# Kernel tuning notes

Measured on AMD Instinct MI355X. Metric: run time of the kernel, lower is better.

The kernel has to match this reference:

```python
import jax, jax.numpy as jnp
import numpy as np

EPS = 1e-5
ALPHA = 0.05   # propalpha
GDEP = 2       # gcn_depth
LAYERS = 3     # gcn_layers
NUM_TCN = 2    # num_layer tcn units per encoder


def conv1x1(W, b, x):
    # 1x1 Conv2d on [B,C,N,1]: pure channel mix
    return jnp.einsum('oc,bcnl->bonl', W, x) + b[None, :, None, None]


def tcn_unit(Wf, bf, Wg, bg, h):
    # gated TCN unit: tanh(filter) * sigmoid(gate), 1x1 convs (L==1)
    return jnp.tanh(conv1x1(Wf, bf, h)) * jax.nn.sigmoid(conv1x1(Wg, bg, h))


def mixprop(x, A, W, b):
    # MTGNN mixprop: add self-loops, row-normalize, gdep propagation steps,
    # concat hops on channel dim, 1x1 conv mlp. A: [N,N] or [B,N,N].
    N = A.shape[-1]
    A = A + jnp.eye(N, dtype=A.dtype)
    A = A / A.sum(-1, keepdims=True)
    h = x
    outs = [h]
    for _ in range(GDEP):
        if A.ndim == 2:
            hn = jnp.einsum('vw,bcwl->bcvl', A, h)
        else:
            hn = jnp.einsum('bvw,bcwl->bcvl', A, h)
        h = ALPHA * x + (1.0 - ALPHA) * hn
        outs.append(h)
    ho = jnp.concatenate(outs, axis=1)  # [B,(GDEP+1)*C,N,1]
    return conv1x1(W, b, ho)


def layernorm(x, w, b):
    # LayerNorm over (C,N,1) of [B,C,N,1]; idx=arange(N) selects full affine
    mu = x.mean(axis=(1, 2, 3), keepdims=True)
    var = x.var(axis=(1, 2, 3), keepdims=True)
    return (x - mu) / jnp.sqrt(var + EPS) * w[None] + b[None]


def setup_inputs() -> dict:
    key = jax.random.key(0)
    B, N, E, H, S, T = 8, 2048, 32, 128, 256, 12
    ks = jax.random.split(key, 32)
    s = 0.05
    inp = {
        'x': jax.random.normal(ks[0], (B, E, N, 1), jnp.float32),
        'dy_graph': jax.random.uniform(ks[1], (B, N, N), jnp.float32),
        'static_graph': jax.random.uniform(ks[2], (N, N), jnp.float32),
        'spatial_emb': jax.random.normal(ks[3], (B, 32, N, 1), jnp.float32),
        'temporal_d_emb': jax.random.normal(ks[4], (B, 32, N, 1), jnp.float32),
        'temporal_w_emb': jax.random.normal(ks[5], (B, 32, N, 1), jnp.float32),
        'enc_Wf': s * jax.random.normal(ks[6], (LAYERS, NUM_TCN, H, H), jnp.float32),
        'enc_bf': s * jax.random.normal(ks[7], (LAYERS, NUM_TCN, H), jnp.float32),
        'enc_Wg': s * jax.random.normal(ks[8], (LAYERS, NUM_TCN, H, H), jnp.float32),
        'enc_bg': s * jax.random.normal(ks[9], (LAYERS, NUM_TCN, H), jnp.float32),
        'skip_W': s * jax.random.normal(ks[10], (LAYERS, S, H), jnp.float32),
        'skip_b': s * jax.random.normal(ks[11], (LAYERS, S), jnp.float32),
        'norm_w': jnp.ones((LAYERS, E, N, 1), jnp.float32),
        'norm_b': jnp.zeros((LAYERS, E, N, 1), jnp.float32),
        'g0_W': s * jax.random.normal(ks[12], (LAYERS, E, (GDEP + 1) * E), jnp.float32),
        'g0_b': s * jax.random.normal(ks[13], (LAYERS, E), jnp.float32),
        'g1_W': s * jax.random.normal(ks[14], (LAYERS, E, (GDEP + 1) * E), jnp.float32),
        'g1_b': s * jax.random.normal(ks[15], (LAYERS, E), jnp.float32),
        'g2_W': s * jax.random.normal(ks[16], (LAYERS, E, (GDEP + 1) * E), jnp.float32),
        'g2_b': s * jax.random.normal(ks[17], (LAYERS, E), jnp.float32),
        'skipE_W': s * jax.random.normal(ks[18], (S, E), jnp.float32),
        'skipE_b': s * jax.random.normal(ks[19], (S,), jnp.float32),
        'end_W': s * jax.random.normal(ks[20], (T, S), jnp.float32),
        'end_b': s * jax.random.normal(ks[21], (T,), jnp.float32),
    }
    return inp


def reference(x, dy_graph, static_graph, spatial_emb, temporal_d_emb, temporal_w_emb,
              enc_Wf, enc_bf, enc_Wg, enc_bg, skip_W, skip_b, norm_w, norm_b,
              g0_W, g0_b, g1_W, g1_b, g2_W, g2_b, skipE_W, skipE_b, end_W, end_b):
    adp = dy_graph
    skip = 0.0
    for i in range(LAYERS):
        residual = x
        hidden = jnp.concatenate([x, spatial_emb, temporal_d_emb, temporal_w_emb], axis=1)
        for j in range(NUM_TCN):
            hidden = tcn_unit(enc_Wf[i, j], enc_bf[i, j], enc_Wg[i, j], enc_bg[i, j], hidden)
        skip = conv1x1(skip_W[i], skip_b[i], hidden) + skip
        x = (mixprop(x, static_graph, g0_W[i], g0_b[i])
             + mixprop(x, adp, g1_W[i], g1_b[i])
             + mixprop(x, jnp.swapaxes(adp, -1, -2), g2_W[i], g2_b[i]))
        x = x + residual
        x = jax.nn.relu(layernorm(x, norm_w[i], norm_b[i]))
    skip = conv1x1(skipE_W, skipE_b, x) + skip
    return conv1x1(end_W, end_b, skip)  # [B, seq_length, N, 1]
```

## Files before the change

### kernel.cpp

```cpp
#include <hip/hip_runtime.h>
#include <stdint.h>


typedef uint16_t u16;
typedef uint32_t u32;
typedef __attribute__((ext_vector_type(8))) short s8v;
typedef __attribute__((ext_vector_type(4))) float f4v;

#define MFMA16(a,b,c) __builtin_amdgcn_mfma_f32_16x16x32_bf16(a,b,c,0,0,0)

__device__ __forceinline__ float b2f(u16 u){ union{u32 i; float f;} x; x.i=(u32)u<<16; return x.f; }
__device__ __forceinline__ u16 f2b(float f){
  u32 u = __builtin_bit_cast(u32, f);
  u32 r = (u + 0x7fffu + ((u >> 16) & 1u)) >> 16;
  return (u16)r;
}

__device__ __forceinline__ void gld16(const void* g, void* l) {
  __builtin_amdgcn_global_load_lds(
      (const __attribute__((address_space(1))) void*)g,
      (__attribute__((address_space(3))) void*)l, 16, 0, 0);
}

__global__ __launch_bounds__(256) void kdetect(const u16* __restrict__ x, int* __restrict__ flag)
{
  const int i = blockIdx.x*256 + threadIdx.x;
  const uint4 v = ((const uint4*)x)[i];
  const u32 w[4] = {v.x, v.y, v.z, v.w};
  int cnt = 0;
  #pragma unroll
  for (int e = 0; e < 4; e++) {
    if ((w[e] & 0x7F80u) == 0x7F80u) cnt++;
    if (((w[e] >> 16) & 0x7F80u) == 0x7F80u) cnt++;
  }
  const unsigned long long m = __ballot(cnt != 0);
  if (m && (threadIdx.x & 63) == 0) atomicOr(flag, 1);
}

__global__ __launch_bounds__(256) void kcvt4(const void* __restrict__ src, u16* __restrict__ dst,
                                             int n4, const int* __restrict__ flag)
{
  if (!*flag) return;
  const int i = blockIdx.x*256 + threadIdx.x;
  if (i >= n4) return;
  const float4 v = ((const float4*)src)[i];
  u16 o[4]; o[0]=f2b(v.x); o[1]=f2b(v.y); o[2]=f2b(v.z); o[3]=f2b(v.w);
  *(uint2*)(dst + (long)i*4) = *(uint2*)o;
}

struct CvtTab { const void* s[18]; u16* d[18]; int n4[18]; };
__global__ __launch_bounds__(256) void kcvt_small(CvtTab tb, const int* __restrict__ flag)
{
  const int e = blockIdx.y;
  const int i = blockIdx.x*256 + threadIdx.x;
  if (i >= tb.n4[e]) return;
  if (*flag) {
    const float4 v = ((const float4*)tb.s[e])[i];
    u16 o[4]; o[0]=f2b(v.x); o[1]=f2b(v.y); o[2]=f2b(v.z); o[3]=f2b(v.w);
    *(uint2*)(tb.d[e] + (long)i*4) = *(uint2*)o;
  } else {
    *(uint2*)(tb.d[e] + (long)i*4) = ((const uint2*)tb.s[e])[i];
  }
}

__global__ __launch_bounds__(256) void kcvtT(
    const void* __restrict__ src, u16* __restrict__ dyb, u16* __restrict__ dytb,
    float* __restrict__ rsum, float* __restrict__ csum, const int* __restrict__ flag)
{
  __shared__ alignas(16) u32 tt[64][32];
  const int tid = threadIdx.x;
  const int b = blockIdx.z;
  const long r0 = (long)blockIdx.y*64;
  const long c0 = (long)blockIdx.x*64;
  const int rp = tid>>3, c8 = (tid&7)*8;
  const long base = (long)b*4194304;
  const int fl = *flag;

  u16 lo[8], hi[8];
  const long gl = base + (r0 + 2*rp)*2048 + c0 + c8;
  const long gh = gl + 2048;
  if (fl) {
    const float* sl = (const float*)src + gl;
    const float* sh = (const float*)src + gh;
    const float4 a0 = ((const float4*)sl)[0], a1 = ((const float4*)sl)[1];
    const float4 b0 = ((const float4*)sh)[0], b1 = ((const float4*)sh)[1];
    lo[0]=f2b(a0.x); lo[1]=f2b(a0.y); lo[2]=f2b(a0.z); lo[3]=f2b(a0.w);
    lo[4]=f2b(a1.x); lo[5]=f2b(a1.y); lo[6]=f2b(a1.z); lo[7]=f2b(a1.w);
    hi[0]=f2b(b0.x); hi[1]=f2b(b0.y); hi[2]=f2b(b0.z); hi[3]=f2b(b0.w);
    hi[4]=f2b(b1.x); hi[5]=f2b(b1.y); hi[6]=f2b(b1.z); hi[7]=f2b(b1.w);
    *(uint4*)(dyb + gl) = *(uint4*)lo;
    *(uint4*)(dyb + gh) = *(uint4*)hi;
  } else {
    *(uint4*)lo = *((const uint4*)((const u16*)src + gl));
    *(uint4*)hi = *((const uint4*)((const u16*)src + gh));
  }
  float rsl = 0.f, rsh = 0.f;
  #pragma unroll
  for (int e = 0; e < 8; e++) {
    rsl += b2f(lo[e]); rsh += b2f(hi[e]);
    const int c = c8 + e;
    tt[c][rp ^ ((c & 0x38) >> 1)] = (u32)lo[e] | ((u32)hi[e] << 16);
  }
  rsl += __shfl_down(rsl, 4, 8); rsl += __shfl_down(rsl, 2, 8); rsl += __shfl_down(rsl, 1, 8);
  rsh += __shfl_down(rsh, 4, 8); rsh += __shfl_down(rsh, 2, 8); rsh += __shfl_down(rsh, 1, 8);
  if ((tid & 7) == 0) {
    atomicAdd(rsum + b*2048 + r0 + 2*rp,     rsl);
    atomicAdd(rsum + b*2048 + r0 + 2*rp + 1, rsh);
  }
  __syncthreads();

  const int c = tid>>2, j4 = (tid&3)*8;
  const int sw = (c & 0x38) >> 1;
  u32 q[8];
  *(uint4*)&q[0] = *(const uint4*)&tt[c][j4 ^ sw];
  *(uint4*)&q[4] = *(const uint4*)&tt[c][(j4 + 4) ^ sw];
  float cs = 0.f;
  #pragma unroll
  for (int e = 0; e < 8; e++) { cs += b2f((u16)q[e]); cs += b2f((u16)(q[e] >> 16)); }
  cs += __shfl_down(cs, 2, 4); cs += __shfl_down(cs, 1, 4);
  u16* dp = dytb + base + (c0 + c)*2048 + r0 + 2*j4;
  *(uint4*)(dp)     = *(uint4*)&q[0];
  *(uint4*)(dp + 8) = *(uint4*)&q[4];
  if ((tid & 3) == 0) atomicAdd(csum + b*2048 + c0 + c, cs);
}

__global__ void kfin(float* __restrict__ v){
  const int i = blockIdx.x*256 + threadIdx.x;
  v[i] = 1.f/(1.f + v[i]);
}

struct PG {
  const u16* Ac0; const u16* Ac1; const u16* Ac2;
  const u16* Ar0; const u16* Ar1;
  const int* flag;
  long ab0, ab1, ab2;
  const u16* X0; const u16* X1; const u16* X2;
  const float* R0; const float* R1; const float* R2;
  long rb0, rb1, rb2;
  u16* O0; u16* O1; u16* O2;
};

__global__ __launch_bounds__(256) void kprops(PG p, long x_bs, long o_bs)
{
  __shared__ u16 Al[4][64][64];
  __shared__ u16 Xl[4][32][64];
  const int tid = threadIdx.x, wave = tid>>6, lane = tid&63;
  const int lw = lane&15, quad = lane>>4;
  const int wr = wave>>1, wc = wave&1;
  const int v0 = blockIdx.x*64;
  const int b = blockIdx.y, g = blockIdx.z;
  const int fl = *p.flag;
  const u16* Ag; long ab; const u16* Xg; const float* Rg; long rb; u16* Og;
  if (g == 0)      { Ag = fl ? p.Ac0 : p.Ar0; ab = p.ab0; Xg = p.X0; Rg = p.R0; rb = p.rb0; Og = p.O0; }
  else if (g == 1) { Ag = fl ? p.Ac1 : p.Ar1; ab = p.ab1; Xg = p.X1; Rg = p.R1; rb = p.rb1; Og = p.O1; }
  else             { Ag = p.Ac2;              ab = p.ab2; Xg = p.X2; Rg = p.R2; rb = p.rb2; Og = p.O2; }
  const u16* Ab = Ag + (long)b*ab;
  const u16* Xb = Xg + (long)b*x_bs;

  const int srow = wave*8 + (lane>>3);
  const int skc  = lane&7;
  const long soff = (long)((skc ^ (srow&7))*8);
  const u16* srcA0 = Ab + (long)(v0 + srow)*2048 + soff;
  const u16* srcA1 = Ab + (long)(v0 + 32 + srow)*2048 + soff;
  const u16* srcX  = Xb + (long)srow*2048 + soff;

#define STAGE(tt) do { const int bb_=(tt)&3; const long k0_=(long)(tt)*64;          \
    gld16(srcA0 + k0_, (void*)((char*)&Al[bb_][0][0]  + wave*1024));                \
    gld16(srcA1 + k0_, (void*)((char*)&Al[bb_][32][0] + wave*1024));                \
    gld16(srcX  + k0_, (void*)((char*)&Xl[bb_][0][0]  + wave*1024)); } while(0)

  f4v acc0 = {0.f,0.f,0.f,0.f}, acc1 = {0.f,0.f,0.f,0.f};
  const int arow0 = wr*32 + lw;
  const int arow1 = wr*32 + 16 + lw;
  const int xrow  = wc*16 + lw;
  const int sw    = lw & 7;
  const int q0    = (quad ^ sw)*8;
  const int q1    = ((quad ^ sw) ^ 4)*8;

  STAGE(0); STAGE(1); STAGE(2);

  #pragma unroll 1
  for (int t = 0; t < 32; t++) {
    if (t < 30)       asm volatile("s_waitcnt vmcnt(6)" ::: "memory");
    else if (t == 30) asm volatile("s_waitcnt vmcnt(3)" ::: "memory");
    else              asm volatile("s_waitcnt vmcnt(0)" ::: "memory");
    __builtin_amdgcn_s_barrier();
    __builtin_amdgcn_sched_barrier(0);
    const int bb = t&3;
    s8v x0  = *(const s8v*)&Xl[bb][xrow][q0];
    s8v a00 = *(const s8v*)&Al[bb][arow0][q0];
    s8v a10 = *(const s8v*)&Al[bb][arow1][q0];
    s8v x1  = *(const s8v*)&Xl[bb][xrow][q1];
    s8v a01 = *(const s8v*)&Al[bb][arow0][q1];
    s8v a11 = *(const s8v*)&Al[bb][arow1][q1];
    acc0 = MFMA16(a00, x0, acc0);
    acc1 = MFMA16(a10, x0, acc1);
    acc0 = MFMA16(a01, x1, acc0);
    acc1 = MFMA16(a11, x1, acc1);
    if (t <= 28) STAGE(t+3);
  }
#undef STAGE

  const int c = wc*16 + lw;
  const float* rp = Rg + (long)b*rb;
  u16* ob = Og + (long)b*o_bs;
  #pragma unroll
  for (int f = 0; f < 2; f++) {
    const f4v s = f ? acc1 : acc0;
    const int vb = v0 + wr*32 + f*16 + quad*4;
    const u16* dp = Xb + (long)c*2048 + vb;
    u16 pk[4];
    #pragma unroll
    for (int r = 0; r < 4; r++) pk[r] = f2b((s[r] + b2f(dp[r])) * rp[vb + r]);
    *(uint2*)(ob + (long)c*2048 + vb) = *(uint2*)pk;
  }
}

template<int TRANSA, int MODE>
__global__ __launch_bounds__(256) void kprop(
    const u16* __restrict__ A, long a_bs, int lda, int K,
    const u16* __restrict__ X, long x_bs, int ldx,
    const u16* __restrict__ D, long d_bs,
    const float* __restrict__ rinv, long r_bs,
    const float* __restrict__ bias,
    u16* __restrict__ out0, float* __restrict__ out1, long o_bs,
    float* __restrict__ stats)
{
  __shared__ u16 As[4][2][16][40];
  __shared__ f4v red[4][2][64];
  const int tid = threadIdx.x;
  const int wave = tid >> 6, lane = tid & 63;
  const int lw = lane & 15, quad = lane >> 4;
  const int v0 = blockIdx.x * 16;
  const int ball = blockIdx.z + blockIdx.y;
  const u16* Ab = A + (long)ball * a_bs;
  const u16* Xb = X + (long)ball * x_bs;
  const int KC = K >> 5;

  f4v acc0 = {0.f,0.f,0.f,0.f}, acc1 = {0.f,0.f,0.f,0.f};

  int r0, c0_;
  if (TRANSA == 0) { r0 = lane >> 2; c0_ = (lane & 3) * 8; }
  else             { r0 = lane >> 1; c0_ = (lane & 1) * 8; }

  int ci = wave;
  bool has = ci < KC;
  uint4 d = make_uint4(0,0,0,0);
  if (has) {
    d = (TRANSA == 0)
      ? *(const uint4*)(Ab + (long)(v0 + r0) * lda + ci * 32 + c0_)
      : *(const uint4*)(Ab + (long)(ci * 32 + r0) * lda + v0 + c0_);
  }
  int buf = 0;
  while (has) {
    if (TRANSA == 0) {
      *(uint4*)&As[wave][buf][r0][c0_] = d;
    } else {
      u16 tmp[8]; *(uint4*)tmp = d;
      #pragma unroll
      for (int e = 0; e < 8; e++) As[wave][buf][c0_ + e][r0] = tmp[e];
    }
    const int cn = ci + 4;
    const bool hn = cn < KC;
    if (hn) {
      d = (TRANSA == 0)
        ? *(const uint4*)(Ab + (long)(v0 + r0) * lda + cn * 32 + c0_)
        : *(const uint4*)(Ab + (long)(cn * 32 + r0) * lda + v0 + c0_);
    }
    s8v af = *(const s8v*)&As[wave][buf][lw][quad * 8];
    const u16* xk = Xb + ci * 32 + quad * 8;
    s8v b0 = *(const s8v*)(xk + (long)lw * ldx);
    s8v b1 = *(const s8v*)(xk + (long)(16 + lw) * ldx);
    acc0 = MFMA16(af, b0, acc0);
    acc1 = MFMA16(af, b1, acc1);
    ci = cn; has = hn; buf ^= 1;
  }
  red[wave][0][lane] = acc0;
  red[wave][1][lane] = acc1;
  __syncthreads();
  if (wave == 0) {
    const int vb = v0 + quad * 4;
    float ssum = 0.f, sq = 0.f;
    #pragma unroll
    for (int nt = 0; nt < 2; nt++) {
      f4v a = red[0][nt][lane] + red[1][nt][lane] + red[2][nt][lane] + red[3][nt][lane];
      const int c = nt * 16 + lw;
      const u16* dp = D + (long)ball * d_bs + (long)c * 2048 + vb;
      if (MODE == 0) {
        const float* rp = rinv + (long)ball * r_bs + vb;
        u16 pk[4];
        #pragma unroll
        for (int r = 0; r < 4; r++) pk[r] = f2b((a[r] + b2f(dp[r])) * rp[r]);
        *(uint2*)(out0 + (long)ball * o_bs + (long)c * 2048 + vb) = *(uint2*)pk;
      } else {
        const float bs = bias[c];
        float4 st;
        st.x = a[0] + bs + b2f(dp[0]);
        st.y = a[1] + bs + b2f(dp[1]);
        st.z = a[2] + bs + b2f(dp[2]);
        st.w = a[3] + bs + b2f(dp[3]);
        *(float4*)(out1 + (long)ball * o_bs + (long)c * 2048 + vb) = st;
        ssum += st.x + st.y + st.z + st.w;
        sq   += st.x*st.x + st.y*st.y + st.z*st.z + st.w*st.w;
      }
    }
    if (MODE == 1) {
      #pragma unroll
      for (int off = 32; off; off >>= 1) {
        ssum += __shfl_down(ssum, off, 64);
        sq   += __shfl_down(sq,   off, 64);
      }
      if (lane == 0) {
        atomicAdd(stats + ball*2,     ssum);
        atomicAdd(stats + ball*2 + 1, sq);
      }
    }
  }
}

__global__ __launch_bounds__(256) void ktcn2(
    const u16* __restrict__ H,
    const u16* __restrict__ Wf1, const u16* __restrict__ bf1v,
    const u16* __restrict__ Wg1, const u16* __restrict__ bg1v,
    const u16* __restrict__ Wf2, const u16* __restrict__ bf2v,
    const u16* __restrict__ Wg2, const u16* __restrict__ bg2v,
    u16* __restrict__ out)
{
  __shared__ u16 h1[4][16][136];
  const int tid = threadIdx.x, wave = tid>>6, lane = tid&63, lw = lane&15, quad = lane>>4;
  const long j0 = (long)blockIdx.x*64 + wave*16;
  const f4v zero = {0.f,0.f,0.f,0.f};
  f4v accf[8], accg[8];
  #pragma unroll
  for (int nt=0; nt<8; nt++){ accf[nt] = zero; accg[nt] = zero; }
  const u16* Arow = H + (j0 + lw)*128 + quad*8;
  #pragma unroll
  for (int k0 = 0; k0 < 128; k0 += 32) {
    s8v a = *(const s8v*)(Arow + k0);
    #pragma unroll
    for (int nt = 0; nt < 8; nt++) {
      const int o = nt*16 + lw;
      s8v bf_ = *(const s8v*)(Wf1 + o*128 + k0 + quad*8);
      s8v bg_ = *(const s8v*)(Wg1 + o*128 + k0 + quad*8);
      accf[nt] = MFMA16(a, bf_, accf[nt]);
      accg[nt] = MFMA16(a, bg_, accg[nt]);
    }
  }
  #pragma unroll
  for (int nt = 0; nt < 8; nt++) {
    const int o = nt*16 + lw;
    const float fb = b2f(bf1v[o]), gb = b2f(bg1v[o]);
    #pragma unroll
    for (int rr = 0; rr < 4; rr++) {
      const float f = accf[nt][rr] + fb, g = accg[nt][rr] + gb;
      const float e2 = __expf(2.f*f);
      const float th = 1.f - 2.f/(e2 + 1.f);
      const float sg = 1.f/(1.f + __expf(-g));
      h1[wave][quad*4 + rr][o] = f2b(th*sg);
    }
  }
  __syncthreads();
  #pragma unroll
  for (int nt=0; nt<8; nt++){ accf[nt] = zero; accg[nt] = zero; }
  #pragma unroll
  for (int k0 = 0; k0 < 128; k0 += 32) {
    s8v a = *(const s8v*)&h1[wave][lw][k0 + quad*8];
    #pragma unroll
    for (int nt = 0; nt < 8; nt++) {
      const int o = nt*16 + lw;
      s8v bf_ = *(const s8v*)(Wf2 + o*128 + k0 + quad*8);
      s8v bg_ = *(const s8v*)(Wg2 + o*128 + k0 + quad*8);
      accf[nt] = MFMA16(a, bf_, accf[nt]);
      accg[nt] = MFMA16(a, bg_, accg[nt]);
    }
  }
  #pragma unroll
  for (int nt = 0; nt < 8; nt++) {
    const int o = nt*16 + lw;
    const float fb = b2f(bf2v[o]), gb = b2f(bg2v[o]);
    #pragma unroll
    for (int rr = 0; rr < 4; rr++) {
      const long j = j0 + quad*4 + rr;
      const float f = accf[nt][rr] + fb, g = accg[nt][rr] + gb;
      const float e2 = __expf(2.f*f);
      const float th = 1.f - 2.f/(e2 + 1.f);
      const float sg = 1.f/(1.f + __expf(-g));
      out[j*128 + o] = f2b(th*sg);
    }
  }
}

__global__ __launch_bounds__(256) void kskip(
    const u16* __restrict__ A, int lda, int K,
    const u16* __restrict__ W, int ldb,
    const u16* __restrict__ bias,
    float* __restrict__ skipbuf, int addprev, int mode, u16* __restrict__ outb)
{
  const int tid = threadIdx.x, wave = tid>>6, lane = tid&63, lw = lane&15, quad = lane>>4;
  const long j0 = (long)blockIdx.x*64 + wave*16;
  const f4v zero = {0.f,0.f,0.f,0.f};
  f4v acc[16];
  #pragma unroll
  for (int nt=0; nt<16; nt++) acc[nt] = zero;
  const u16* Arow = A + (j0 + lw)*(long)lda + quad*8;
  for (int k0 = 0; k0 < K; k0 += 32) {
    s8v a = *(const s8v*)(Arow + k0);
    #pragma unroll
    for (int nt = 0; nt < 16; nt++) {
      const int o = nt*16 + lw;
      s8v b = *(const s8v*)(W + (long)o*ldb + k0 + quad*8);
      acc[nt] = MFMA16(a, b, acc[nt]);
    }
  }
  #pragma unroll
  for (int nt = 0; nt < 16; nt++) {
    const int o = nt*16 + lw;
    const float bv = b2f(bias[o]);
    #pragma unroll
    for (int rr = 0; rr < 4; rr++) {
      const long j = j0 + quad*4 + rr;
      float v = acc[nt][rr] + bv;
      if (addprev) v += skipbuf[j*256 + o];
      if (mode == 0) skipbuf[j*256 + o] = v;
      else           outb[j*256 + o] = f2b(v);
    }
  }
}

__global__ __launch_bounds__(256) void kend(
    const u16* __restrict__ A, const u16* __restrict__ W, const u16* __restrict__ bias,
    void* __restrict__ outv, const int* __restrict__ flag)
{
  const int tid = threadIdx.x, wave = tid>>6, lane = tid&63, lw = lane&15, quad = lane>>4;
  const long j0 = (long)blockIdx.x*64 + wave*16;
  f4v acc = {0.f,0.f,0.f,0.f};
  const u16* Arow = A + (j0 + lw)*256 + quad*8;
  #pragma unroll
  for (int k0 = 0; k0 < 256; k0 += 32) {
    s8v a = *(const s8v*)(Arow + k0);
    s8v b = {0,0,0,0,0,0,0,0};
    if (lw < 12) b = *(const s8v*)(W + lw*256 + k0 + quad*8);
    acc = MFMA16(a, b, acc);
  }
  if (lw < 12) {
    const float bv = b2f(bias[lw]);
    const int fl = *flag;
    #pragma unroll
    for (int rr = 0; rr < 4; rr++) {
      const long j = j0 + quad*4 + rr;
      const long oi = (j >> 11)*24576 + lw*2048 + (j & 2047);
      const float val = acc[rr] + bv;
      if (fl) ((float*)outv)[oi] = val;
      else    ((u16*)outv)[oi]   = f2b(val);
    }
  }
}

__global__ __launch_bounds__(256) void khid0(
    const void* __restrict__ x, const void* __restrict__ spat,
    const void* __restrict__ tde, const void* __restrict__ twe,
    u16* __restrict__ hid, u16* __restrict__ slot0, const int* __restrict__ flag)
{
  __shared__ u16 t[32][72];
  const int tid = threadIdx.x, b = blockIdx.y, v0 = blockIdx.x*64;
  const int fl = *flag;
  const void* srcs[4] = {x, spat, tde, twe};
  #pragma unroll
  for (int e = 0; e < 4; e++) {
    const int c = tid>>3, v8 = (tid&7)*8;
    const long boff = (long)c*2048 + v0 + v8;
    u16 o8[8];
    if (fl) {
      const float* sp = (const float*)srcs[e] + (long)b*65536 + boff;
      const float4 a = ((const float4*)sp)[0], bb = ((const float4*)sp)[1];
      o8[0]=f2b(a.x); o8[1]=f2b(a.y); o8[2]=f2b(a.z); o8[3]=f2b(a.w);
      o8[4]=f2b(bb.x); o8[5]=f2b(bb.y); o8[6]=f2b(bb.z); o8[7]=f2b(bb.w);
    } else {
      *(uint4*)o8 = *(const uint4*)((const u16*)srcs[e] + (long)b*65536 + boff);
    }
    if (e == 0) *(uint4*)(slot0 + (long)b*458752 + boff) = *(uint4*)o8;
    *(uint4*)&t[c][v8] = *(uint4*)o8;
    __syncthreads();
    const int jl = tid>>2, c8 = (tid&3)*8;
    u16 q8[8];
    #pragma unroll
    for (int i = 0; i < 8; i++) q8[i] = t[c8 + i][jl];
    *(uint4*)(hid + ((long)b*2048 + v0 + jl)*128 + e*32 + c8) = *(uint4*)q8;
    __syncthreads();
  }
}

__global__ __launch_bounds__(256) void krowsum(const u16* __restrict__ srcA, const u16* __restrict__ srcB,
                                               const int* __restrict__ flag,
                                               float* __restrict__ outv, int nrows)
{
  const u16* src = (*flag) ? srcA : srcB;
  const int wave = threadIdx.x>>6, lane = threadIdx.x&63;
  const int row = blockIdx.x*4 + wave;
  if (row >= nrows) return;
  const u16* p = src + (long)row*2048 + lane*8;
  float s = 0.f;
  #pragma unroll
  for (int it = 0; it < 4; it++) {
    u16 v[8]; *(uint4*)v = *(const uint4*)(p + it*512);
    #pragma unroll
    for (int e = 0; e < 8; e++) s += b2f(v[e]);
  }
  #pragma unroll
  for (int off = 32; off; off >>= 1) s += __shfl_down(s, off, 64);
  if (lane == 0) outv[row] = 1.f/(1.f + s);
}

__global__ __launch_bounds__(256) void kweff(
    const u16* __restrict__ g0W, const u16* __restrict__ g1W, const u16* __restrict__ g2W,
    const u16* __restrict__ g0b, const u16* __restrict__ g1b, const u16* __restrict__ g2b,
    u16* __restrict__ weffA, float* __restrict__ bwA)
{
  const int L = blockIdx.y;
  const int ioff = L*3072, boff = L*32;
  u16* weff = weffA + L*7168;
  float* bw = bwA + L*32;
  const int idx = blockIdx.x*256 + threadIdx.x;
  if (idx < 32) bw[idx] = b2f(g0b[boff+idx]) + b2f(g1b[boff+idx]) + b2f(g2b[boff+idx]);
  if (idx >= 7168) return;
  const int o = idx / 224, m = idx % 224;
  const u16* Ws[3] = {g0W + ioff, g1W + ioff, g2W + ioff};
  float val;
  if (m < 32) {
    val = 0.f;
    #pragma unroll
    for (int g = 0; g < 3; g++) {
      const float w0 = b2f(Ws[g][o*96 + m]);
      const float w1 = b2f(Ws[g][o*96 + 32 + m]);
      const float w2 = b2f(Ws[g][o*96 + 64 + m]);
      val += w0 + 0.05f*(w1 + w2);
    }
  } else {
    const int f = (m - 32) >> 5, cc = m & 31;
    const int g = f >> 1, typ = f & 1;
    const float w1 = b2f(Ws[g][o*96 + 32 + cc]);
    const float w2 = b2f(Ws[g][o*96 + 64 + cc]);
    val = (typ == 0) ? (0.95f*w1 + 0.0475f*w2) : (0.9025f*w2);
  }
  weff[o*224 + m] = f2b(val);
}

__global__ __launch_bounds__(256) void kapply(
    const float* __restrict__ xpre, const float* __restrict__ raw,
    const u16* __restrict__ nw, const u16* __restrict__ nb,
    u16* __restrict__ slot0, u16* __restrict__ hid)
{
  __shared__ u16 t[32][72];
  const int tid = threadIdx.x, b = blockIdx.y, v0 = blockIdx.x*64;
  const float mu = raw[b*2] * (1.f/65536.f);
  const float var = raw[b*2+1] * (1.f/65536.f) - mu*mu;
  const float rs = rsqrtf(var + 1e-5f);
  const int c = tid>>3, v8 = (tid&7)*8;
  const long boff = (long)c*2048 + v0 + v8;
  float4 xa = *(const float4*)(xpre + (long)b*65536 + boff);
  float4 xbv = *(const float4*)(xpre + (long)b*65536 + boff + 4);
  u16 wv[8], bv[8], o8[8];
  *(uint4*)wv = *(const uint4*)(nw + boff);
  *(uint4*)bv = *(const uint4*)(nb + boff);
  const float xs[8] = {xa.x, xa.y, xa.z, xa.w, xbv.x, xbv.y, xbv.z, xbv.w};
  #pragma unroll
  for (int e = 0; e < 8; e++) {
    float y = (xs[e] - mu) * rs * b2f(wv[e]) + b2f(bv[e]);
    y = fmaxf(y, 0.f);
    o8[e] = f2b(y);
    t[c][v8 + e] = o8[e];
  }
  *(uint4*)(slot0 + (long)b*458752 + boff) = *(uint4*)o8;
  __syncthreads();
  const int jl = tid>>2, c8 = (tid&3)*8;
  u16 q8[8];
  #pragma unroll
  for (int e = 0; e < 8; e++) q8[e] = t[c8 + e][jl];
  *(uint4*)(hid + ((long)b*2048 + v0 + jl)*128 + c8) = *(uint4*)q8;
}

extern "C" void kernel_launch(void* const* d_in, const int* in_sizes, int n_in,
                              void* d_out, int out_size, void* d_ws, size_t ws_size,
                              hipStream_t stream)
{
  (void)in_sizes; (void)n_in; (void)out_size; (void)ws_size;

  char* ws = (char*)d_ws;
  u16*   pbuf = (u16*)(ws + 0);
  u16*   hid  = (u16*)(ws + 7340032);
  u16*   hb2  = (u16*)(ws + 15728640);
  float* skip = (float*)(ws + 19922944);
  u16*   xsb  = (u16*)(ws + 36700160);
  float* xpre = (float*)(ws + 45088768);
  float* rst  = (float*)(ws + 47203328);
  float* rdy  = (float*)(ws + 47211520);
  float* cdy  = (float*)(ws + 47277056);
  int*   flag = (int*)(ws + 47343616);
  float* raw  = (float*)(ws + 47343744);

  size_t coff = 50331648;
  auto alloc = [&](size_t elems) -> u16* {
    u16* p = (u16*)(ws + coff);
    coff += ((elems*2 + 255)/256)*256;
    return p;
  };
  u16* dyb   = alloc(33554432);
  u16* stgb  = alloc(4194304);
  u16* encWf = alloc(98304);
  u16* encbf = alloc(768);
  u16* encWg = alloc(98304);
  u16* encbg = alloc(768);
  u16* skW   = alloc(98304);
  u16* skb   = alloc(768);
  u16* nw    = alloc(196608);
  u16* nb    = alloc(196608);
  u16* g0W   = alloc(9216);
  u16* g0b   = alloc(96);
  u16* g1W   = alloc(9216);
  u16* g1b   = alloc(96);
  u16* g2W   = alloc(9216);
  u16* g2b   = alloc(96);
  u16* sEW   = alloc(8192);
  u16* sEb   = alloc(256);
  u16* eW    = alloc(3072);
  u16* eb    = alloc(12);
  u16* dytb  = alloc(33554432);
  u16* weffA = alloc(21504);
  float* bwA = (float*)alloc(192);

  hipMemsetAsync(flag, 0, 320, stream);
  hipLaunchKernelGGL(kdetect, dim3(32), dim3(256), 0, stream, (const u16*)d_in[0], flag);

  CvtTab tb;
  {
    const void* ss[18] = { d_in[6], d_in[7], d_in[8], d_in[9], d_in[10], d_in[11],
      d_in[12], d_in[13], d_in[14], d_in[15], d_in[16], d_in[17], d_in[18], d_in[19],
      d_in[20], d_in[21], d_in[22], d_in[23] };
    u16* dd[18] = { encWf, encbf, encWg, encbg, skW, skb, nw, nb,
      g0W, g0b, g1W, g1b, g2W, g2b, sEW, sEb, eW, eb };
    const int nn[18] = { 24576, 192, 24576, 192, 24576, 192, 49152, 49152,
      2304, 24, 2304, 24, 2304, 24, 2048, 64, 768, 3 };
    for (int e = 0; e < 18; e++) { tb.s[e] = ss[e]; tb.d[e] = dd[e]; tb.n4[e] = nn[e]; }
  }
  hipLaunchKernelGGL(kcvt_small, dim3(192, 18), dim3(256), 0, stream, tb, flag);
  hipLaunchKernelGGL(kcvt4, dim3(4096), dim3(256), 0, stream, d_in[2], stgb, 1048576, flag);
  hipLaunchKernelGGL(kweff, dim3(28, 3), dim3(256), 0, stream,
      g0W, g1W, g2W, g0b, g1b, g2b, weffA, bwA);

  hipMemsetAsync(rdy, 0, 131072, stream);
  hipLaunchKernelGGL(kcvtT, dim3(32,32,8), dim3(256), 0, stream,
      d_in[1], dyb, dytb, rdy, cdy, flag);
  hipLaunchKernelGGL(kfin, dim3(128), dim3(256), 0, stream, rdy);
  hipLaunchKernelGGL(krowsum, dim3(512), dim3(256), 0, stream,
      stgb, (const u16*)d_in[2], flag, rst, 2048);
  hipLaunchKernelGGL(khid0, dim3(32,8), dim3(256), 0, stream,
      d_in[0], d_in[3], d_in[4], d_in[5], hid, pbuf, flag);

  const long PB = 458752;
  const long SL = 65536;
  const long DYB = 4194304;

  for (int i = 0; i < 3; i++) {
    hipLaunchKernelGGL(ktcn2, dim3(256), dim3(256), 0, stream,
        hid,
        encWf + (i*2+0)*16384, encbf + (i*2+0)*128, encWg + (i*2+0)*16384, encbg + (i*2+0)*128,
        encWf + (i*2+1)*16384, encbf + (i*2+1)*128, encWg + (i*2+1)*16384, encbg + (i*2+1)*128,
        hb2);
    hipLaunchKernelGGL(kskip, dim3(256), dim3(256), 0, stream,
        hb2, 128, 128, skW + i*32768, 128, skb + i*256, skip, (i>0)?1:0, 0, (u16*)nullptr);

    PG p1;
    p1.Ac0 = stgb; p1.Ac1 = dyb; p1.Ac2 = dytb;
    p1.Ar0 = (const u16*)d_in[2]; p1.Ar1 = (const u16*)d_in[1];
    p1.flag = flag;
    p1.ab0 = 0;   p1.ab1 = DYB; p1.ab2 = DYB;
    p1.X0 = pbuf; p1.X1 = pbuf; p1.X2 = pbuf;
    p1.R0 = rst;  p1.R1 = rdy;  p1.R2 = cdy;
    p1.rb0 = 0;   p1.rb1 = 2048; p1.rb2 = 2048;
    p1.O0 = pbuf + 1*SL; p1.O1 = pbuf + 3*SL; p1.O2 = pbuf + 5*SL;
    hipLaunchKernelGGL(kprops, dim3(32,8,3), dim3(256), 0, stream, p1, PB, PB);

    PG p2 = p1;
    p2.X0 = pbuf + 1*SL; p2.X1 = pbuf + 3*SL; p2.X2 = pbuf + 5*SL;
    p2.O0 = pbuf + 2*SL; p2.O1 = pbuf + 4*SL; p2.O2 = pbuf + 6*SL;
    hipLaunchKernelGGL(kprops, dim3(32,8,3), dim3(256), 0, stream, p2, PB, PB);

    hipLaunchKernelGGL((kprop<1,1>), dim3(128,1,8), dim3(256), 0, stream,
        pbuf, PB, 2048, 224, weffA + i*7168, 0L, 224, pbuf, PB,
        (const float*)nullptr, 0L, bwA + i*32, (u16*)nullptr, xpre, 65536L, raw + i*16);
    hipLaunchKernelGGL(kapply, dim3(32,8), dim3(256), 0, stream,
        xpre, raw + i*16, nw + i*65536, nb + i*65536, pbuf, hid);
  }
  hipLaunchKernelGGL(kskip, dim3(256), dim3(256), 0, stream,
      hid, 128, 32, sEW, 32, sEb, skip, 1, 1, xsb);
  hipLaunchKernelGGL(kend, dim3(256), dim3(256), 0, stream, xsb, eW, eb, d_out, flag);
}
```

Before: 773.3 us.

## Unfuse the two TCN units and widen kcvtT tiles to 128 columns

Replaces the fused two-stage gated TCN kernel with a single-stage kernel launched twice, staging the intermediate activation in a new global buffer instead of shared memory. The dynamic-graph convert/transpose kernel now has each block handle two 64-column tiles, halving the grid and doubling its LDS use. Splitting the TCN adds a global round trip of the intermediate hidden tensor and an extra launch, in exchange for a simpler kernel with no shared memory or barrier. Wider transpose blocks cut block count and amortise per-block setup, but may lower occupancy.

```diff
diff --git a/kernel.cpp b/kernel.cpp
--- a/kernel.cpp
+++ b/kernel.cpp
@@ -67,39 +67,42 @@
     const void* __restrict__ src, u16* __restrict__ dyb, u16* __restrict__ dytb,
     float* __restrict__ rsum, float* __restrict__ csum, const int* __restrict__ flag)
 {
-  __shared__ alignas(16) u32 tt[64][32];
+  __shared__ alignas(16) u32 tt[2][64][32];
   const int tid = threadIdx.x;
   const int b = blockIdx.z;
   const long r0 = (long)blockIdx.y*64;
-  const long c0 = (long)blockIdx.x*64;
-  const int rp = tid>>3, c8 = (tid&7)*8;
+  const long c0 = (long)blockIdx.x*128;
+  const int rp = tid>>3, cg8 = (tid&7)*8;
   const long base = (long)b*4194304;
   const int fl = *flag;
 
-  u16 lo[8], hi[8];
-  const long gl = base + (r0 + 2*rp)*2048 + c0 + c8;
-  const long gh = gl + 2048;
-  if (fl) {
-    const float* sl = (const float*)src + gl;
-    const float* sh = (const float*)src + gh;
-    const float4 a0 = ((const float4*)sl)[0], a1 = ((const float4*)sl)[1];
-    const float4 b0 = ((const float4*)sh)[0], b1 = ((const float4*)sh)[1];
-    lo[0]=f2b(a0.x); lo[1]=f2b(a0.y); lo[2]=f2b(a0.z); lo[3]=f2b(a0.w);
-    lo[4]=f2b(a1.x); lo[5]=f2b(a1.y); lo[6]=f2b(a1.z); lo[7]=f2b(a1.w);
-    hi[0]=f2b(b0.x); hi[1]=f2b(b0.y); hi[2]=f2b(b0.z); hi[3]=f2b(b0.w);
-    hi[4]=f2b(b1.x); hi[5]=f2b(b1.y); hi[6]=f2b(b1.z); hi[7]=f2b(b1.w);
-    *(uint4*)(dyb + gl) = *(uint4*)lo;
-    *(uint4*)(dyb + gh) = *(uint4*)hi;
-  } else {
-    *(uint4*)lo = *((const uint4*)((const u16*)src + gl));
-    *(uint4*)hi = *((const uint4*)((const u16*)src + gh));
-  }
   float rsl = 0.f, rsh = 0.f;
   #pragma unroll
-  for (int e = 0; e < 8; e++) {
-    rsl += b2f(lo[e]); rsh += b2f(hi[e]);
-    const int c = c8 + e;
-    tt[c][rp ^ ((c & 0x38) >> 1)] = (u32)lo[e] | ((u32)hi[e] << 16);
+  for (int h = 0; h < 2; h++) {
+    u16 lo[8], hi[8];
+    const long gl = base + (r0 + 2*rp)*2048 + c0 + h*64 + cg8;
+    const long gh = gl + 2048;
+    if (fl) {
+      const float* sl = (const float*)src + gl;
+      const float* sh = (const float*)src + gh;
+      const float4 a0 = ((const float4*)sl)[0], a1 = ((const float4*)sl)[1];
+      const float4 b0 = ((const float4*)sh)[0], b1 = ((const float4*)sh)[1];
+      lo[0]=f2b(a0.x); lo[1]=f2b(a0.y); lo[2]=f2b(a0.z); lo[3]=f2b(a0.w);
+      lo[4]=f2b(a1.x); lo[5]=f2b(a1.y); lo[6]=f2b(a1.z); lo[7]=f2b(a1.w);
+      hi[0]=f2b(b0.x); hi[1]=f2b(b0.y); hi[2]=f2b(b0.z); hi[3]=f2b(b0.w);
+      hi[4]=f2b(b1.x); hi[5]=f2b(b1.y); hi[6]=f2b(b1.z); hi[7]=f2b(b1.w);
+      *(uint4*)(dyb + gl) = *(uint4*)lo;
+      *(uint4*)(dyb + gh) = *(uint4*)hi;
+    } else {
+      *(uint4*)lo = *((const uint4*)((const u16*)src + gl));
+      *(uint4*)hi = *((const uint4*)((const u16*)src + gh));
+    }
+    #pragma unroll
+    for (int e = 0; e < 8; e++) {
+      rsl += b2f(lo[e]); rsh += b2f(hi[e]);
+      const int c = cg8 + e;
+      tt[h][c][rp ^ ((c & 0x38) >> 1)] = (u32)lo[e] | ((u32)hi[e] << 16);
+    }
   }
   rsl += __shfl_down(rsl, 4, 8); rsl += __shfl_down(rsl, 2, 8); rsl += __shfl_down(rsl, 1, 8);
   rsh += __shfl_down(rsh, 4, 8); rsh += __shfl_down(rsh, 2, 8); rsh += __shfl_down(rsh, 1, 8);
@@ -109,19 +112,22 @@
   }
   __syncthreads();
 
-  const int c = tid>>2, j4 = (tid&3)*8;
-  const int sw = (c & 0x38) >> 1;
-  u32 q[8];
-  *(uint4*)&q[0] = *(const uint4*)&tt[c][j4 ^ sw];
-  *(uint4*)&q[4] = *(const uint4*)&tt[c][(j4 + 4) ^ sw];
-  float cs = 0.f;
-  #pragma unroll
-  for (int e = 0; e < 8; e++) { cs += b2f((u16)q[e]); cs += b2f((u16)(q[e] >> 16)); }
-  cs += __shfl_down(cs, 2, 4); cs += __shfl_down(cs, 1, 4);
-  u16* dp = dytb + base + (c0 + c)*2048 + r0 + 2*j4;
-  *(uint4*)(dp)     = *(uint4*)&q[0];
-  *(uint4*)(dp + 8) = *(uint4*)&q[4];
-  if ((tid & 3) == 0) atomicAdd(csum + b*2048 + c0 + c, cs);
+  #pragma unroll
+  for (int h = 0; h < 2; h++) {
+    const int c = tid>>2, j4 = (tid&3)*8;
+    const int sw = (c & 0x38) >> 1;
+    u32 q[8];
+    *(uint4*)&q[0] = *(const uint4*)&tt[h][c][j4 ^ sw];
+    *(uint4*)&q[4] = *(const uint4*)&tt[h][c][(j4 + 4) ^ sw];
+    float cs = 0.f;
+    #pragma unroll
+    for (int e = 0; e < 8; e++) { cs += b2f((u16)q[e]); cs += b2f((u16)(q[e] >> 16)); }
+    cs += __shfl_down(cs, 2, 4); cs += __shfl_down(cs, 1, 4);
+    u16* dp = dytb + base + (c0 + h*64 + c)*2048 + r0 + 2*j4;
+    *(uint4*)(dp)     = *(uint4*)&q[0];
+    *(uint4*)(dp + 8) = *(uint4*)&q[4];
+    if ((tid & 3) == 0) atomicAdd(csum + b*2048 + c0 + h*64 + c, cs);
+  }
 }
 
 __global__ void kfin(float* __restrict__ v){
@@ -318,15 +324,10 @@
   }
 }
 
-__global__ __launch_bounds__(256) void ktcn2(
-    const u16* __restrict__ H,
-    const u16* __restrict__ Wf1, const u16* __restrict__ bf1v,
-    const u16* __restrict__ Wg1, const u16* __restrict__ bg1v,
-    const u16* __restrict__ Wf2, const u16* __restrict__ bf2v,
-    const u16* __restrict__ Wg2, const u16* __restrict__ bg2v,
-    u16* __restrict__ out)
-{
-  __shared__ u16 h1[4][16][136];
+__global__ __launch_bounds__(256) void ktcn(
+    const u16* __restrict__ H, const u16* __restrict__ Wf, const u16* __restrict__ bfv,
+    const u16* __restrict__ Wg, const u16* __restrict__ bgv, u16* __restrict__ out)
+{
   const int tid = threadIdx.x, wave = tid>>6, lane = tid&63, lw = lane&15, quad = lane>>4;
   const long j0 = (long)blockIdx.x*64 + wave*16;
   const f4v zero = {0.f,0.f,0.f,0.f};
@@ -340,8 +341,8 @@
     #pragma unroll
     for (int nt = 0; nt < 8; nt++) {
       const int o = nt*16 + lw;
-      s8v bf_ = *(const s8v*)(Wf1 + o*128 + k0 + quad*8);
-      s8v bg_ = *(const s8v*)(Wg1 + o*128 + k0 + quad*8);
+      s8v bf_ = *(const s8v*)(Wf + o*128 + k0 + quad*8);
+      s8v bg_ = *(const s8v*)(Wg + o*128 + k0 + quad*8);
       accf[nt] = MFMA16(a, bf_, accf[nt]);
       accg[nt] = MFMA16(a, bg_, accg[nt]);
     }
@@ -349,35 +350,7 @@
   #pragma unroll
   for (int nt = 0; nt < 8; nt++) {
     const int o = nt*16 + lw;
-    const float fb = b2f(bf1v[o]), gb = b2f(bg1v[o]);
-    #pragma unroll
-    for (int rr = 0; rr < 4; rr++) {
-      const float f = accf[nt][rr] + fb, g = accg[nt][rr] + gb;
-      const float e2 = __expf(2.f*f);
-      const float th = 1.f - 2.f/(e2 + 1.f);
-      const float sg = 1.f/(1.f + __expf(-g));
-      h1[wave][quad*4 + rr][o] = f2b(th*sg);
-    }
-  }
-  __syncthreads();
-  #pragma unroll
-  for (int nt=0; nt<8; nt++){ accf[nt] = zero; accg[nt] = zero; }
-  #pragma unroll
-  for (int k0 = 0; k0 < 128; k0 += 32) {
-    s8v a = *(const s8v*)&h1[wave][lw][k0 + quad*8];
-    #pragma unroll
-    for (int nt = 0; nt < 8; nt++) {
-      const int o = nt*16 + lw;
-      s8v bf_ = *(const s8v*)(Wf2 + o*128 + k0 + quad*8);
-      s8v bg_ = *(const s8v*)(Wg2 + o*128 + k0 + quad*8);
-      accf[nt] = MFMA16(a, bf_, accf[nt]);
-      accg[nt] = MFMA16(a, bg_, accg[nt]);
-    }
-  }
-  #pragma unroll
-  for (int nt = 0; nt < 8; nt++) {
-    const int o = nt*16 + lw;
-    const float fb = b2f(bf2v[o]), gb = b2f(bg2v[o]);
+    const float fb = b2f(bfv[o]), gb = b2f(bgv[o]);
     #pragma unroll
     for (int rr = 0; rr < 4; rr++) {
       const long j = j0 + quad*4 + rr;
@@ -588,6 +561,7 @@
   char* ws = (char*)d_ws;
   u16*   pbuf = (u16*)(ws + 0);
   u16*   hid  = (u16*)(ws + 7340032);
+  u16*   hb1  = (u16*)(ws + 11534336);
   u16*   hb2  = (u16*)(ws + 15728640);
   float* skip = (float*)(ws + 19922944);
   u16*   xsb  = (u16*)(ws + 36700160);
@@ -648,7 +622,7 @@
       g0W, g1W, g2W, g0b, g1b, g2b, weffA, bwA);
 
   hipMemsetAsync(rdy, 0, 131072, stream);
-  hipLaunchKernelGGL(kcvtT, dim3(32,32,8), dim3(256), 0, stream,
+  hipLaunchKernelGGL(kcvtT, dim3(16,32,8), dim3(256), 0, stream,
       d_in[1], dyb, dytb, rdy, cdy, flag);
   hipLaunchKernelGGL(kfin, dim3(128), dim3(256), 0, stream, rdy);
   hipLaunchKernelGGL(krowsum, dim3(512), dim3(256), 0, stream,
@@ -661,11 +635,10 @@
   const long DYB = 4194304;
 
   for (int i = 0; i < 3; i++) {
-    hipLaunchKernelGGL(ktcn2, dim3(256), dim3(256), 0, stream,
-        hid,
-        encWf + (i*2+0)*16384, encbf + (i*2+0)*128, encWg + (i*2+0)*16384, encbg + (i*2+0)*128,
-        encWf + (i*2+1)*16384, encbf + (i*2+1)*128, encWg + (i*2+1)*16384, encbg + (i*2+1)*128,
-        hb2);
+    hipLaunchKernelGGL(ktcn, dim3(256), dim3(256), 0, stream,
+        hid, encWf + (i*2+0)*16384, encbf + (i*2+0)*128, encWg + (i*2+0)*16384, encbg + (i*2+0)*128, hb1);
+    hipLaunchKernelGGL(ktcn, dim3(256), dim3(256), 0, stream,
+        hb1, encWf + (i*2+1)*16384, encbf + (i*2+1)*128, encWg + (i*2+1)*16384, encbg + (i*2+1)*128, hb2);
     hipLaunchKernelGGL(kskip, dim3(256), dim3(256), 0, stream,
         hb2, 128, 128, skW + i*32768, 128, skb + i*256, skip, (i>0)?1:0, 0, (u16*)nullptr);
 
```

Result: no change. 773.1 us (-0.0%).
